# Kernel optimization log

Measured on AMD Instinct MI355X. Metric: run time of the kernel, lower is better.

The kernel has to match this reference:

```python
import jax, jax.numpy as jnp
import numpy as np

D_MODEL = 1024
NUM_HEADS = 16
HEAD_DIM = D_MODEL // NUM_HEADS
B, S = 4, 2048


def setup_inputs() -> dict:
    key = jax.random.key(0)
    ks = jax.random.split(key, 11)
    sc = 1.0 / np.sqrt(D_MODEL)
    return {
        "query": jax.random.normal(ks[0], (B, S, D_MODEL), jnp.float32),
        "key": jax.random.normal(ks[1], (B, S, D_MODEL), jnp.float32),
        "value": jax.random.normal(ks[2], (B, S, D_MODEL), jnp.float32),
        "Wq": jax.random.normal(ks[3], (D_MODEL, D_MODEL), jnp.float32) * sc,
        "bq": jnp.zeros((D_MODEL,), jnp.float32),
        "Wk": jax.random.normal(ks[4], (D_MODEL, D_MODEL), jnp.float32) * sc,
        "bk": jnp.zeros((D_MODEL,), jnp.float32),
        "Wv": jax.random.normal(ks[5], (D_MODEL, D_MODEL), jnp.float32) * sc,
        "bv": jnp.zeros((D_MODEL,), jnp.float32),
        "Wo": jax.random.normal(ks[6], (D_MODEL, D_MODEL), jnp.float32) * sc,
        "bo": jnp.zeros((D_MODEL,), jnp.float32),
    }


def _split_heads(x):
    b, s, _ = x.shape
    return x.reshape(b, s, NUM_HEADS, HEAD_DIM).transpose(0, 2, 1, 3)  # [B,H,S,Dh]


def reference(query, key, value, Wq, bq, Wk, bk, Wv, bv, Wo, bo):
    q = _split_heads(query @ Wq + bq)
    k = _split_heads(key @ Wk + bk)
    v = _split_heads(value @ Wv + bv)
    scores = jnp.einsum("bhqd,bhkd->bhqk", q, k) / np.sqrt(HEAD_DIM)
    attn = jax.nn.softmax(scores, axis=-1)
    out = jnp.einsum("bhqk,bhkd->bhqd", attn, v)
    out = out.transpose(0, 2, 1, 3).reshape(query.shape[0], -1, D_MODEL)
    return out @ Wo + bo
```

## Files before the change

kernel.cpp:

```cpp
#include <hip/hip_runtime.h>

typedef unsigned short u16;
typedef unsigned int   u32;
typedef unsigned long long u64;
typedef __attribute__((ext_vector_type(8))) short bf16x8;
typedef __attribute__((ext_vector_type(4))) float f32x4;

#define S_  2048
#define DH  64
#define DM  1024
#define BS  8192
#define CS  0.18033688011112042f

static __device__ __forceinline__ float bf2f(u16 v){ return __uint_as_float(((u32)v)<<16); }
static __device__ __forceinline__ u16 f2bf(float f){
  u32 x = __float_as_uint(f);
  return (u16)((x + 0x7fffu + ((x>>16)&1u)) >> 16);
}
#if __has_builtin(__builtin_amdgcn_cvt_pk_bf16_f32)
static __device__ __forceinline__ u32 pk2(float x, float y){
  typedef __attribute__((ext_vector_type(2))) __bf16 bf2v;
  union { bf2v v; u32 u; } c; c.v = __builtin_amdgcn_cvt_pk_bf16_f32(x, y); return c.u;
}
#else
static __device__ __forceinline__ u32 pk2(float x, float y){
  return (u32)f2bf(x) | ((u32)f2bf(y) << 16);
}
#endif
#if __has_builtin(__builtin_amdgcn_exp2f)
#define EXP2F(x) __builtin_amdgcn_exp2f(x)
#else
#define EXP2F(x) exp2f(x)
#endif

static __device__ __forceinline__ void dma16(const u16* g, const u16* l){
  __builtin_amdgcn_global_load_lds(
      (const __attribute__((address_space(1))) u32*)(u64)(uintptr_t)g,
      (__attribute__((address_space(3))) u32*)(u32)(u64)(uintptr_t)l, 16, 0, 0);
}

static __device__ __forceinline__ bf16x8 lds_frag(const u16* p){
  union { bf16x8 f; uint2 u[2]; } w;
  w.u[0] = *(const uint2*)(p);
  w.u[1] = *(const uint2*)(p+4);
  return w.f;
}
static __device__ __forceinline__ bf16x8 frag16v(const u16* p){
  union { bf16x8 f; uint4 u; } w;
  w.u = *(const uint4*)p;
  return w.f;
}
static __device__ __forceinline__ void stage16_bf(const u16* __restrict__ g, u16* s){
  uint4 a = *(const uint4*)g;
  uint4 b = *(const uint4*)(g+8);
  *(uint2*)(s+0)  = make_uint2(a.x,a.y);
  *(uint2*)(s+4)  = make_uint2(a.z,a.w);
  *(uint2*)(s+8)  = make_uint2(b.x,b.y);
  *(uint2*)(s+12) = make_uint2(b.z,b.w);
}
static __device__ __forceinline__ void stage16_f32(const float* __restrict__ g, u16* s){
  float4 a0 = ((const float4*)g)[0];
  float4 a1 = ((const float4*)g)[1];
  float4 a2 = ((const float4*)g)[2];
  float4 a3 = ((const float4*)g)[3];
  *(uint2*)(s+0)  = make_uint2(pk2(a0.x,a0.y), pk2(a0.z,a0.w));
  *(uint2*)(s+4)  = make_uint2(pk2(a1.x,a1.y), pk2(a1.z,a1.w));
  *(uint2*)(s+8)  = make_uint2(pk2(a2.x,a2.y), pk2(a2.z,a2.w));
  *(uint2*)(s+12) = make_uint2(pk2(a3.x,a3.y), pk2(a3.z,a3.w));
}

__global__ __launch_bounds__(256) void prep(
    const void* __restrict__ w0, const void* __restrict__ w1,
    const void* __restrict__ w2, const void* __restrict__ w3,
    u16* t0, u16* t1, u16* t2, u16* t3,
    const void* __restrict__ a0, const void* __restrict__ a1,
    const void* __restrict__ a2,
    u16* c0, u16* c1, u16* c2, const int f32f){
  __shared__ u16 tile[32][33];
  int z = blockIdx.z;
  int tid = threadIdx.x;
  bool f32 = f32f != 0;
  if (z < 4){
    const void* in = z==0?w0 : z==1?w1 : z==2?w2 : w3;
    u16* out = z==0?t0 : z==1?t1 : z==2?t2 : t3;
    int tx = tid & 31, ty = tid >> 5;
    int c  = blockIdx.x*32 + tx;
    int r0 = blockIdx.y*32;
    for (int i=ty;i<32;i+=8){
      long off = (long)(r0+i)*DM + c;
      tile[i][tx] = f32 ? f2bf(((const float*)in)[off]) : ((const u16*)in)[off];
    }
    __syncthreads();
    int rr = r0 + tx, cb = blockIdx.x*32;
    for (int i=ty;i<32;i+=8) out[(long)(cb+i)*DM + rr] = tile[tx][i];
  } else {
    if (!f32) return;
    const void* in = z==4?a0 : z==5?a1 : a2;
    u16* out = z==4?c0 : z==5?c1 : c2;
    long lb = (long)blockIdx.y*32 + blockIdx.x;
    long base = (lb*256 + tid)*8;
    #pragma unroll
    for (int it=0; it<4; it++){
      long i = base + (long)it*2097152;
      const float4* p = (const float4*)((const float*)in + i);
      float4 x = p[0], y = p[1];
      *(uint4*)(out + i) = make_uint4(pk2(x.x,x.y), pk2(x.z,x.w), pk2(y.x,y.y), pk2(y.z,y.w));
    }
  }
}

template<int ADMA>
__global__ __launch_bounds__(256) void gemm_qkv(
    const void* __restrict__ A0, const void* __restrict__ A1, const void* __restrict__ A2,
    const u16* __restrict__ W0, const u16* __restrict__ W1, const u16* __restrict__ W2,
    const void* __restrict__ bv0, const void* __restrict__ bv1, const void* __restrict__ bv2,
    u16* C0, u16* C1, u16* C2, const int f32f){
  constexpr int AST = ADMA ? 32 : 36;
  constexpr int NB  = ADMA ? 2 : 1;
  __shared__ __align__(16) u16 As[NB][128*AST];
  __shared__ __align__(16) u16 Bs[NB][128*32];
  int z = blockIdx.z;
  const void* A  = z==0?A0 : z==1?A1 : A2;
  const u16* BT  = z==0?W0 : z==1?W1 : W2;
  const void* bias = z==0?bv0 : z==1?bv1 : bv2;
  u16* C = z==0?C0 : z==1?C1 : C2;
  const bool aF32 = (!ADMA) && (f32f != 0);
  const bool bF32 = (f32f != 0);
  int tid = threadIdx.x;
  int bx = blockIdx.y;
  int lane = tid & 63, w = tid >> 6;
  int t = lane & 15, q = lane >> 4;
  int wr = w >> 1, wc = w & 1;

  const u16* gB = BT + ((long)(bx*128 + w*32 + (lane>>2))*DM + (lane&3)*8);
  float scale = (z==0) ? CS : 1.0f;

  for (int sub = 0; sub < 2; ++sub){
    int by = blockIdx.x*2 + sub;
    f32x4 acc[4][4];
    #pragma unroll
    for(int i=0;i<4;i++) for(int j=0;j<4;j++) for(int k=0;k<4;k++) acc[i][j][k]=0.f;

    if constexpr (ADMA){
      const u16* gA = (const u16*)A + ((long)(by*128 + w*32 + (lane>>2))*DM + (lane&3)*8);
      const int lb = (w*32)*32;
      dma16(gA,         &As[0][lb]);
      dma16(gA + 16*DM, &As[0][lb + 16*32]);
      dma16(gB,         &Bs[0][lb]);
      dma16(gB + 16*DM, &Bs[0][lb + 16*32]);
      for (int k0=0; k0<DM; k0+=32){
        int cur = (k0>>5)&1;
        if (k0+32 < DM){
          dma16(gA + k0+32,         &As[cur^1][lb]);
          dma16(gA + k0+32 + 16*DM, &As[cur^1][lb + 16*32]);
          dma16(gB + k0+32,         &Bs[cur^1][lb]);
          dma16(gB + k0+32 + 16*DM, &Bs[cur^1][lb + 16*32]);
          asm volatile("s_waitcnt vmcnt(4)" ::: "memory");
        } else {
          asm volatile("s_waitcnt vmcnt(0)" ::: "memory");
        }
        __builtin_amdgcn_s_barrier();
        bf16x8 af[4], bfr[4];
        const u16* Ar = &As[cur][(wr*64 + t)*32 + q*8];
        const u16* Br = &Bs[cur][(wc*64 + t)*32 + q*8];
        #pragma unroll
        for (int rt=0;rt<4;rt++) af[rt]  = frag16v(Ar + rt*16*32);
        #pragma unroll
        for (int ct=0;ct<4;ct++) bfr[ct] = frag16v(Br + ct*16*32);
        #pragma unroll
        for (int rt=0;rt<4;rt++)
          #pragma unroll
          for (int ct=0;ct<4;ct++)
            acc[rt][ct] = __builtin_amdgcn_mfma_f32_16x16x32_bf16(af[rt], bfr[ct], acc[rt][ct], 0,0,0);
        __builtin_amdgcn_s_barrier();
      }
    } else {
      long aoff = (long)(by*128 + (tid>>1))*DM + (tid&1)*16;
      const u16* ArdB = &As[0][(wr*64 + t)*AST + q*8];
      const u16* BrdB = &Bs[0][(wc*64 + t)*32  + q*8];
      for (int k0=0; k0<DM; k0+=32){
        dma16(gB + k0,         &Bs[0][(w*32)*32]);
        dma16(gB + 16*DM + k0, &Bs[0][(w*32)*32 + 16*32]);
        u16* AsW = &As[0][(tid>>1)*36 + (tid&1)*16];
        if (aF32) stage16_f32((const float*)A + aoff + k0, AsW);
        else      stage16_bf ((const u16*)A  + aoff + k0, AsW);
        __syncthreads();
        bf16x8 af[4], bfr[4];
        #pragma unroll
        for (int rt=0;rt<4;rt++) af[rt]  = lds_frag(ArdB + rt*16*AST);
        #pragma unroll
        for (int ct=0;ct<4;ct++) bfr[ct] = lds_frag(BrdB + ct*16*32);
        #pragma unroll
        for (int rt=0;rt<4;rt++)
          #pragma unroll
          for (int ct=0;ct<4;ct++)
            acc[rt][ct] = __builtin_amdgcn_mfma_f32_16x16x32_bf16(af[rt], bfr[ct], acc[rt][ct], 0,0,0);
        __syncthreads();
      }
    }

    #pragma unroll
    for (int ct=0;ct<4;ct++){
      int col = bx*128 + wc*64 + ct*16 + t;
      float bvv = bF32 ? ((const float*)bias)[col] : bf2f(((const u16*)bias)[col]);
      #pragma unroll
      for (int rt=0;rt<4;rt++){
        int row0 = by*128 + wr*64 + rt*16 + q*4;
        if (z == 2){
          int bb = row0 >> 11, s = row0 & 2047;
          long vbase = (long)bb*2097152 + (long)col*2048
                     + (s & ~63) + ((rt>>1)<<5) + (q<<3) + ((rt&1)<<2);
          u32 lo = pk2(acc[rt][ct][0]+bvv, acc[rt][ct][1]+bvv);
          u32 hi = pk2(acc[rt][ct][2]+bvv, acc[rt][ct][3]+bvv);
          *(uint2*)(C + vbase) = make_uint2(lo,hi);
        } else {
          #pragma unroll
          for (int r=0;r<4;r++)
            C[(long)(row0+r)*DM + col] = f2bf((acc[rt][ct][r] + bvv)*scale);
        }
      }
    }
  }
}

__global__ __launch_bounds__(256) void gemm_o(const u16* __restrict__ A,
    const u16* __restrict__ BT, const void* __restrict__ bias, void* __restrict__ C,
    const int f32f){
  __shared__ __align__(16) u16 As[2][128*32];
  __shared__ __align__(16) u16 Bs[2][128*32];
  const int f = f32f;
  int tid = threadIdx.x;
  int by = blockIdx.x, bx = blockIdx.y;
  int lane = tid & 63, w = tid >> 6;
  int t = lane & 15, q = lane >> 4;
  int wr = w >> 1, wc = w & 1;
  f32x4 acc[4][4];
  #pragma unroll
  for(int i=0;i<4;i++) for(int j=0;j<4;j++) for(int k=0;k<4;k++) acc[i][j][k]=0.f;

  const u16* gA = A  + ((long)(by*128 + w*32 + (lane>>2))*DM + (lane&3)*8);
  const u16* gB = BT + ((long)(bx*128 + w*32 + (lane>>2))*DM + (lane&3)*8);
  const int lb = (w*32)*32;
  dma16(gA,         &As[0][lb]);
  dma16(gA + 16*DM, &As[0][lb + 16*32]);
  dma16(gB,         &Bs[0][lb]);
  dma16(gB + 16*DM, &Bs[0][lb + 16*32]);
  for (int k0=0; k0<DM; k0+=32){
    int cur = (k0>>5)&1;
    if (k0+32 < DM){
      dma16(gA + k0+32,         &As[cur^1][lb]);
      dma16(gA + k0+32 + 16*DM, &As[cur^1][lb + 16*32]);
      dma16(gB + k0+32,         &Bs[cur^1][lb]);
      dma16(gB + k0+32 + 16*DM, &Bs[cur^1][lb + 16*32]);
      asm volatile("s_waitcnt vmcnt(4)" ::: "memory");
    } else {
      asm volatile("s_waitcnt vmcnt(0)" ::: "memory");
    }
    __builtin_amdgcn_s_barrier();
    bf16x8 af[4], bfr[4];
    const u16* Ar = &As[cur][(wr*64 + t)*32 + q*8];
    const u16* Br = &Bs[cur][(wc*64 + t)*32 + q*8];
    #pragma unroll
    for (int rt=0;rt<4;rt++) af[rt]  = frag16v(Ar + rt*16*32);
    #pragma unroll
    for (int ct=0;ct<4;ct++) bfr[ct] = frag16v(Br + ct*16*32);
    #pragma unroll
    for (int rt=0;rt<4;rt++)
      #pragma unroll
      for (int ct=0;ct<4;ct++)
        acc[rt][ct] = __builtin_amdgcn_mfma_f32_16x16x32_bf16(af[rt], bfr[ct], acc[rt][ct], 0,0,0);
    __builtin_amdgcn_s_barrier();
  }
  #pragma unroll
  for (int ct=0;ct<4;ct++){
    int col = bx*128 + wc*64 + ct*16 + t;
    float bvv = f ? ((const float*)bias)[col] : bf2f(((const u16*)bias)[col]);
    #pragma unroll
    for (int rt=0;rt<4;rt++){
      int row0 = by*128 + wr*64 + rt*16 + q*4;
      #pragma unroll
      for (int r=0;r<4;r++){
        long idx = (long)(row0+r)*DM + col;
        float v = acc[rt][ct][r] + bvv;
        if (f) ((float*)C)[idx] = v;
        else   ((u16*)C)[idx]  = f2bf(v);
      }
    }
  }
}

__global__ __launch_bounds__(256,4) void attn5(const u16* __restrict__ Q,
    const u16* __restrict__ Kb, const u16* __restrict__ Vt, u16* __restrict__ O){
  __shared__ __align__(16) u16 Ks[2][4096];
  __shared__ __align__(16) u16 Vs[2][4096];
  int tid = threadIdx.x;
  int bid = blockIdx.x;
  int qt = bid >> 6;
  int s6 = bid & 63;
  int bh = (s6 & 7)*8 + (s6 >> 3);
  int b = bh >> 4, h = bh & 15;
  int lane = tid & 63, w = tid >> 6;
  int t = lane & 15, q = lane >> 4;

  const u16* Qbase = Q + ((long)(b*S_ + qt*128 + w*32 + t)*DM + h*DH + q*8);
  bf16x8 qf[2][2];
  qf[0][0] = frag16v(Qbase);
  qf[0][1] = frag16v(Qbase + 32);
  qf[1][0] = frag16v(Qbase + 16*DM);
  qf[1][1] = frag16v(Qbase + 16*DM + 32);

  int r0 = tid >> 3;
  int cb = ((tid & 7) * 16) ^ ((r0 & 7) << 4);
  const char* gK = (const char*)Kb + (((long)(b*S_ + r0)*DM + h*DH) << 1) + cb;
  const char* gV = (const char*)Vt + ((((long)bh << 17) + ((long)r0 << 11)) << 1) + cb;
  const long gK1 = ((long)32*DM) << 1;
  const long gV1 = ((long)32*S_) << 1;
  const int ld0 = w*512, ld1 = 2048 + w*512;

  f32x4 o[2][4];
  #pragma unroll
  for (int i=0;i<2;i++) for (int j=0;j<4;j++) for (int k=0;k<4;k++) o[i][j][k]=0.f;
  f32x4 o4[2];
  #pragma unroll
  for (int i=0;i<2;i++) for (int k=0;k<4;k++) o4[i][k]=0.f;

  union { bf16x8 f; u32 u[4]; } vone;
  { u32 ovv = (t==0) ? 0x3F803F80u : 0u;
    vone.u[0]=ovv; vone.u[1]=ovv; vone.u[2]=ovv; vone.u[3]=ovv; }

  const int xorv = (t & 7) << 4;

  dma16((const u16*)(gK),       &Ks[0][ld0]);
  dma16((const u16*)(gK + gK1), &Ks[0][ld1]);
  dma16((const u16*)(gV),       &Vs[0][ld0]);
  dma16((const u16*)(gV + gV1), &Vs[0][ld1]);

  for (int kt=0; kt<32; kt++){
    int cur = kt & 1;
    if (kt < 31){
      long ko = ((long)(kt+1)*64*DM) << 1;
      long vo = (long)(kt+1) << 7;
      dma16((const u16*)(gK + ko),       &Ks[cur^1][ld0]);
      dma16((const u16*)(gK + ko + gK1), &Ks[cur^1][ld1]);
      dma16((const u16*)(gV + vo),       &Vs[cur^1][ld0]);
      dma16((const u16*)(gV + vo + gV1), &Vs[cur^1][ld1]);
      asm volatile("s_waitcnt vmcnt(4)" ::: "memory");
    } else {
      asm volatile("s_waitcnt vmcnt(0)" ::: "memory");
    }
    __builtin_amdgcn_s_barrier();

    const u16* Kc = Ks[cur];
    const u16* Vc = Vs[cur];

    f32x4 sacc[2][4];
    #pragma unroll
    for (int i=0;i<2;i++) for (int j=0;j<4;j++) for (int k=0;k<4;k++) sacc[i][j][k]=0.f;
    #pragma unroll
    for (int ks=0; ks<2; ks++){
      int off = ((ks*64 + q*16) ^ xorv) >> 1;
      bf16x8 k0 = frag16v(Kc + (t     )*64 + off);
      bf16x8 k1 = frag16v(Kc + (16 + t)*64 + off);
      bf16x8 k2 = frag16v(Kc + (32 + t)*64 + off);
      bf16x8 k3 = frag16v(Kc + (48 + t)*64 + off);
      __builtin_amdgcn_s_setprio(1);
      #pragma unroll
      for (int rt=0; rt<2; rt++){
        sacc[rt][0] = __builtin_amdgcn_mfma_f32_16x16x32_bf16(k0, qf[rt][ks], sacc[rt][0],0,0,0);
        sacc[rt][1] = __builtin_amdgcn_mfma_f32_16x16x32_bf16(k1, qf[rt][ks], sacc[rt][1],0,0,0);
        sacc[rt][2] = __builtin_amdgcn_mfma_f32_16x16x32_bf16(k2, qf[rt][ks], sacc[rt][2],0,0,0);
        sacc[rt][3] = __builtin_amdgcn_mfma_f32_16x16x32_bf16(k3, qf[rt][ks], sacc[rt][3],0,0,0);
      }
      __builtin_amdgcn_s_setprio(0);
    }

    union { bf16x8 f; u32 u[4]; } af[2][2];
    #pragma unroll
    for (int rt=0; rt<2; rt++){
      float ev[4][4];
      #pragma unroll
      for (int c=0; c<4; c++)
        #pragma unroll
        for (int r=0; r<4; r++) ev[c][r] = EXP2F(sacc[rt][c][r]);
      #pragma unroll
      for (int ks=0; ks<2; ks++){
        af[rt][ks].u[0] = pk2(ev[2*ks  ][0], ev[2*ks  ][1]);
        af[rt][ks].u[1] = pk2(ev[2*ks  ][2], ev[2*ks  ][3]);
        af[rt][ks].u[2] = pk2(ev[2*ks+1][0], ev[2*ks+1][1]);
        af[rt][ks].u[3] = pk2(ev[2*ks+1][2], ev[2*ks+1][3]);
      }
    }

    #pragma unroll
    for (int ks=0; ks<2; ks++){
      int off = ((ks*64 + q*16) ^ xorv) >> 1;
      bf16x8 v0 = frag16v(Vc + (t     )*64 + off);
      bf16x8 v1 = frag16v(Vc + (16 + t)*64 + off);
      bf16x8 v2 = frag16v(Vc + (32 + t)*64 + off);
      bf16x8 v3 = frag16v(Vc + (48 + t)*64 + off);
      __builtin_amdgcn_s_setprio(1);
      #pragma unroll
      for (int rt=0; rt<2; rt++){
        o[rt][0] = __builtin_amdgcn_mfma_f32_16x16x32_bf16(af[rt][ks].f, v0, o[rt][0],0,0,0);
        o[rt][1] = __builtin_amdgcn_mfma_f32_16x16x32_bf16(af[rt][ks].f, v1, o[rt][1],0,0,0);
        o[rt][2] = __builtin_amdgcn_mfma_f32_16x16x32_bf16(af[rt][ks].f, v2, o[rt][2],0,0,0);
        o[rt][3] = __builtin_amdgcn_mfma_f32_16x16x32_bf16(af[rt][ks].f, v3, o[rt][3],0,0,0);
        o4[rt]   = __builtin_amdgcn_mfma_f32_16x16x32_bf16(af[rt][ks].f, vone.f, o4[rt],0,0,0);
      }
      __builtin_amdgcn_s_setprio(0);
    }
    __builtin_amdgcn_s_barrier();
  }

  #pragma unroll
  for (int rt=0; rt<2; rt++){
    #pragma unroll
    for (int r=0; r<4; r++){
      float l = __shfl(o4[rt][r], lane & 48);
      float inv = 1.f / l;
      int row = qt*128 + w*32 + rt*16 + q*4 + r;
      #pragma unroll
      for (int ct=0; ct<4; ct++)
        O[(long)(b*S_ + row)*DM + h*DH + ct*16 + t] = f2bf(o[rt][ct][r] * inv);
    }
  }
}

extern "C" void kernel_launch(void* const* d_in, const int* in_sizes, int n_in,
                              void* d_out, int out_size, void* d_ws, size_t ws_size,
                              hipStream_t stream){
  (void)n_in; (void)out_size;
  const void* xq = d_in[0];
  const void* xk = d_in[1];
  const void* xv = d_in[2];
  const void* Wq = d_in[3];
  const void* bq = d_in[4];
  const void* Wk = d_in[5];
  const void* bk = d_in[6];
  const void* Wv = d_in[7];
  const void* bv = d_in[8];
  const void* Wo = d_in[9];
  const void* bo = d_in[10];

  const long NT = (long)BS*DM;
  int f32f = 1;
  if (in_sizes && in_sizes[0] == (int)(NT*2)) f32f = 0;

  u16* base = (u16*)((char*)d_ws + 256);
  u16* Qb  = base;
  u16* Kbf = base + NT;
  u16* Vt  = base + 2*NT;
  u16* WqT = base + 3*NT;
  u16* WkT = WqT + (long)DM*DM;
  u16* WvT = WkT + (long)DM*DM;
  u16* WoT = WvT + (long)DM*DM;
  u16* Xc0 = WoT + (long)DM*DM;
  u16* Xc1 = Xc0 + NT;
  u16* Xc2 = Xc1 + NT;
  size_t need_pre = 256 + (size_t)(6*NT + 4*(long)DM*DM)*2;
  bool pre = ws_size >= need_pre;

  dim3 gb(256,1,1);
  int nz = (pre && f32f) ? 7 : 4;
  prep<<<dim3(32,32,nz), gb, 0, stream>>>(Wq, Wk, Wv, Wo,
      WqT, WkT, WvT, WoT, xq, xk, xv, Xc0, Xc1, Xc2, f32f);

  if (pre){
    const void* Aq = f32f ? (const void*)Xc0 : xq;
    const void* Ak = f32f ? (const void*)Xc1 : xk;
    const void* Av = f32f ? (const void*)Xc2 : xv;
    gemm_qkv<1><<<dim3(32,8,3), gb, 0, stream>>>(Aq, Ak, Av,
        WqT, WkT, WvT, bq, bk, bv, Qb, Kbf, Vt, f32f);
  } else {
    gemm_qkv<0><<<dim3(32,8,3), gb, 0, stream>>>(xq, xk, xv,
        WqT, WkT, WvT, bq, bk, bv, Qb, Kbf, Vt, f32f);
  }

  attn5<<<dim3(1024,1,1), gb, 0, stream>>>(Qb, Kbf, Vt, Qb );

  gemm_o<<<dim3(64,8,1), gb, 0, stream>>>(Qb, WoT, bo, d_out, f32f);
}
```

Measured before the change: 383.4 us.

## Swizzle LDS tile layout in GEMMs and drop two-tile loop in QKV GEMM

Changes the global-to-LDS DMA address mapping and fragment read offsets to an XOR-swizzled layout in both the QKV and output-projection GEMMs, aiming to remove LDS bank conflicts on the 16-byte fragment reads. The QKV GEMM no longer loops over two row tiles per block. It launches twice as many blocks (64 instead of 32 in x), one tile each, trading weight-tile reuse for more parallelism. The swizzle must match exactly between the DMA writes and the fragment reads for results to stay correct.

```diff
diff --git a/kernel.cpp b/kernel.cpp
--- a/kernel.cpp
+++ b/kernel.cpp
@@ -127,97 +127,96 @@
   const bool aF32 = (!ADMA) && (f32f != 0);
   const bool bF32 = (f32f != 0);
   int tid = threadIdx.x;
-  int bx = blockIdx.y;
+  int by = blockIdx.x, bx = blockIdx.y;
   int lane = tid & 63, w = tid >> 6;
   int t = lane & 15, q = lane >> 4;
   int wr = w >> 1, wc = w & 1;
-
-  const u16* gB = BT + ((long)(bx*128 + w*32 + (lane>>2))*DM + (lane&3)*8);
+  f32x4 acc[4][4];
+  #pragma unroll
+  for(int i=0;i<4;i++) for(int j=0;j<4;j++) for(int k=0;k<4;k++) acc[i][j][k]=0.f;
+
+  if constexpr (ADMA){
+    int sl = (lane & 7) ^ (lane >> 3);
+    int srow = ((lane >> 3) << 1) + (sl >> 2);
+    const u16* gA = (const u16*)A + ((long)(by*128 + w*32 + srow)*DM + (sl&3)*8);
+    const u16* gB = BT            + ((long)(bx*128 + w*32 + srow)*DM + (sl&3)*8);
+    const int lb = w*1024;
+    int rdo = ((t>>1)<<6) + (((((t&1)<<2) | q) ^ (t>>1)) << 3);
+    dma16(gA,         &As[0][lb]);
+    dma16(gA + 16*DM, &As[0][lb + 512]);
+    dma16(gB,         &Bs[0][lb]);
+    dma16(gB + 16*DM, &Bs[0][lb + 512]);
+    for (int k0=0; k0<DM; k0+=32){
+      int cur = (k0>>5)&1;
+      if (k0+32 < DM){
+        dma16(gA + k0+32,         &As[cur^1][lb]);
+        dma16(gA + k0+32 + 16*DM, &As[cur^1][lb + 512]);
+        dma16(gB + k0+32,         &Bs[cur^1][lb]);
+        dma16(gB + k0+32 + 16*DM, &Bs[cur^1][lb + 512]);
+        asm volatile("s_waitcnt vmcnt(4)" ::: "memory");
+      } else {
+        asm volatile("s_waitcnt vmcnt(0)" ::: "memory");
+      }
+      __builtin_amdgcn_s_barrier();
+      bf16x8 af[4], bfr[4];
+      const u16* Ar = &As[cur][wr*2048 + rdo];
+      const u16* Br = &Bs[cur][wc*2048 + rdo];
+      #pragma unroll
+      for (int rt=0;rt<4;rt++) af[rt]  = frag16v(Ar + rt*512);
+      #pragma unroll
+      for (int ct=0;ct<4;ct++) bfr[ct] = frag16v(Br + ct*512);
+      #pragma unroll
+      for (int rt=0;rt<4;rt++)
+        #pragma unroll
+        for (int ct=0;ct<4;ct++)
+          acc[rt][ct] = __builtin_amdgcn_mfma_f32_16x16x32_bf16(af[rt], bfr[ct], acc[rt][ct], 0,0,0);
+      __builtin_amdgcn_s_barrier();
+    }
+  } else {
+    const u16* gB = BT + ((long)(bx*128 + w*32 + (lane>>2))*DM + (lane&3)*8);
+    long aoff = (long)(by*128 + (tid>>1))*DM + (tid&1)*16;
+    const u16* ArdB = &As[0][(wr*64 + t)*AST + q*8];
+    const u16* BrdB = &Bs[0][(wc*64 + t)*32  + q*8];
+    for (int k0=0; k0<DM; k0+=32){
+      dma16(gB + k0,         &Bs[0][w*1024]);
+      dma16(gB + 16*DM + k0, &Bs[0][w*1024 + 512]);
+      u16* AsW = &As[0][(tid>>1)*36 + (tid&1)*16];
+      if (aF32) stage16_f32((const float*)A + aoff + k0, AsW);
+      else      stage16_bf ((const u16*)A  + aoff + k0, AsW);
+      __syncthreads();
+      bf16x8 af[4], bfr[4];
+      #pragma unroll
+      for (int rt=0;rt<4;rt++) af[rt]  = lds_frag(ArdB + rt*16*AST);
+      #pragma unroll
+      for (int ct=0;ct<4;ct++) bfr[ct] = lds_frag(BrdB + ct*16*32);
+      #pragma unroll
+      for (int rt=0;rt<4;rt++)
+        #pragma unroll
+        for (int ct=0;ct<4;ct++)
+          acc[rt][ct] = __builtin_amdgcn_mfma_f32_16x16x32_bf16(af[rt], bfr[ct], acc[rt][ct], 0,0,0);
+      __syncthreads();
+    }
+  }
+
   float scale = (z==0) ? CS : 1.0f;
-
-  for (int sub = 0; sub < 2; ++sub){
-    int by = blockIdx.x*2 + sub;
-    f32x4 acc[4][4];
-    #pragma unroll
-    for(int i=0;i<4;i++) for(int j=0;j<4;j++) for(int k=0;k<4;k++) acc[i][j][k]=0.f;
-
-    if constexpr (ADMA){
-      const u16* gA = (const u16*)A + ((long)(by*128 + w*32 + (lane>>2))*DM + (lane&3)*8);
-      const int lb = (w*32)*32;
-      dma16(gA,         &As[0][lb]);
-      dma16(gA + 16*DM, &As[0][lb + 16*32]);
-      dma16(gB,         &Bs[0][lb]);
-      dma16(gB + 16*DM, &Bs[0][lb + 16*32]);
-      for (int k0=0; k0<DM; k0+=32){
-        int cur = (k0>>5)&1;
-        if (k0+32 < DM){
-          dma16(gA + k0+32,         &As[cur^1][lb]);
-          dma16(gA + k0+32 + 16*DM, &As[cur^1][lb + 16*32]);
-          dma16(gB + k0+32,         &Bs[cur^1][lb]);
-          dma16(gB + k0+32 + 16*DM, &Bs[cur^1][lb + 16*32]);
-          asm volatile("s_waitcnt vmcnt(4)" ::: "memory");
-        } else {
-          asm volatile("s_waitcnt vmcnt(0)" ::: "memory");
-        }
-        __builtin_amdgcn_s_barrier();
-        bf16x8 af[4], bfr[4];
-        const u16* Ar = &As[cur][(wr*64 + t)*32 + q*8];
-        const u16* Br = &Bs[cur][(wc*64 + t)*32 + q*8];
+  #pragma unroll
+  for (int ct=0;ct<4;ct++){
+    int col = bx*128 + wc*64 + ct*16 + t;
+    float bvv = bF32 ? ((const float*)bias)[col] : bf2f(((const u16*)bias)[col]);
+    #pragma unroll
+    for (int rt=0;rt<4;rt++){
+      int row0 = by*128 + wr*64 + rt*16 + q*4;
+      if (z == 2){
+        int bb = row0 >> 11, s = row0 & 2047;
+        long vbase = (long)bb*2097152 + (long)col*2048
+                   + (s & ~63) + ((rt>>1)<<5) + (q<<3) + ((rt&1)<<2);
+        u32 lo = pk2(acc[rt][ct][0]+bvv, acc[rt][ct][1]+bvv);
+        u32 hi = pk2(acc[rt][ct][2]+bvv, acc[rt][ct][3]+bvv);
+        *(uint2*)(C + vbase) = make_uint2(lo,hi);
+      } else {
         #pragma unroll
-        for (int rt=0;rt<4;rt++) af[rt]  = frag16v(Ar + rt*16*32);
-        #pragma unroll
-        for (int ct=0;ct<4;ct++) bfr[ct] = frag16v(Br + ct*16*32);
-        #pragma unroll
-        for (int rt=0;rt<4;rt++)
-          #pragma unroll
-          for (int ct=0;ct<4;ct++)
-            acc[rt][ct] = __builtin_amdgcn_mfma_f32_16x16x32_bf16(af[rt], bfr[ct], acc[rt][ct], 0,0,0);
-        __builtin_amdgcn_s_barrier();
-      }
-    } else {
-      long aoff = (long)(by*128 + (tid>>1))*DM + (tid&1)*16;
-      const u16* ArdB = &As[0][(wr*64 + t)*AST + q*8];
-      const u16* BrdB = &Bs[0][(wc*64 + t)*32  + q*8];
-      for (int k0=0; k0<DM; k0+=32){
-        dma16(gB + k0,         &Bs[0][(w*32)*32]);
-        dma16(gB + 16*DM + k0, &Bs[0][(w*32)*32 + 16*32]);
-        u16* AsW = &As[0][(tid>>1)*36 + (tid&1)*16];
-        if (aF32) stage16_f32((const float*)A + aoff + k0, AsW);
-        else      stage16_bf ((const u16*)A  + aoff + k0, AsW);
-        __syncthreads();
-        bf16x8 af[4], bfr[4];
-        #pragma unroll
-        for (int rt=0;rt<4;rt++) af[rt]  = lds_frag(ArdB + rt*16*AST);
-        #pragma unroll
-        for (int ct=0;ct<4;ct++) bfr[ct] = lds_frag(BrdB + ct*16*32);
-        #pragma unroll
-        for (int rt=0;rt<4;rt++)
-          #pragma unroll
-          for (int ct=0;ct<4;ct++)
-            acc[rt][ct] = __builtin_amdgcn_mfma_f32_16x16x32_bf16(af[rt], bfr[ct], acc[rt][ct], 0,0,0);
-        __syncthreads();
-      }
-    }
-
-    #pragma unroll
-    for (int ct=0;ct<4;ct++){
-      int col = bx*128 + wc*64 + ct*16 + t;
-      float bvv = bF32 ? ((const float*)bias)[col] : bf2f(((const u16*)bias)[col]);
-      #pragma unroll
-      for (int rt=0;rt<4;rt++){
-        int row0 = by*128 + wr*64 + rt*16 + q*4;
-        if (z == 2){
-          int bb = row0 >> 11, s = row0 & 2047;
-          long vbase = (long)bb*2097152 + (long)col*2048
-                     + (s & ~63) + ((rt>>1)<<5) + (q<<3) + ((rt&1)<<2);
-          u32 lo = pk2(acc[rt][ct][0]+bvv, acc[rt][ct][1]+bvv);
-          u32 hi = pk2(acc[rt][ct][2]+bvv, acc[rt][ct][3]+bvv);
-          *(uint2*)(C + vbase) = make_uint2(lo,hi);
-        } else {
-          #pragma unroll
-          for (int r=0;r<4;r++)
-            C[(long)(row0+r)*DM + col] = f2bf((acc[rt][ct][r] + bvv)*scale);
-        }
+        for (int r=0;r<4;r++)
+          C[(long)(row0+r)*DM + col] = f2bf((acc[rt][ct][r] + bvv)*scale);
       }
     }
   }
@@ -238,32 +237,35 @@
   #pragma unroll
   for(int i=0;i<4;i++) for(int j=0;j<4;j++) for(int k=0;k<4;k++) acc[i][j][k]=0.f;
 
-  const u16* gA = A  + ((long)(by*128 + w*32 + (lane>>2))*DM + (lane&3)*8);
-  const u16* gB = BT + ((long)(bx*128 + w*32 + (lane>>2))*DM + (lane&3)*8);
-  const int lb = (w*32)*32;
+  int sl = (lane & 7) ^ (lane >> 3);
+  int srow = ((lane >> 3) << 1) + (sl >> 2);
+  const u16* gA = A  + ((long)(by*128 + w*32 + srow)*DM + (sl&3)*8);
+  const u16* gB = BT + ((long)(bx*128 + w*32 + srow)*DM + (sl&3)*8);
+  const int lb = w*1024;
+  int rdo = ((t>>1)<<6) + (((((t&1)<<2) | q) ^ (t>>1)) << 3);
   dma16(gA,         &As[0][lb]);
-  dma16(gA + 16*DM, &As[0][lb + 16*32]);
+  dma16(gA + 16*DM, &As[0][lb + 512]);
   dma16(gB,         &Bs[0][lb]);
-  dma16(gB + 16*DM, &Bs[0][lb + 16*32]);
+  dma16(gB + 16*DM, &Bs[0][lb + 512]);
   for (int k0=0; k0<DM; k0+=32){
     int cur = (k0>>5)&1;
     if (k0+32 < DM){
       dma16(gA + k0+32,         &As[cur^1][lb]);
-      dma16(gA + k0+32 + 16*DM, &As[cur^1][lb + 16*32]);
+      dma16(gA + k0+32 + 16*DM, &As[cur^1][lb + 512]);
       dma16(gB + k0+32,         &Bs[cur^1][lb]);
-      dma16(gB + k0+32 + 16*DM, &Bs[cur^1][lb + 16*32]);
+      dma16(gB + k0+32 + 16*DM, &Bs[cur^1][lb + 512]);
       asm volatile("s_waitcnt vmcnt(4)" ::: "memory");
     } else {
       asm volatile("s_waitcnt vmcnt(0)" ::: "memory");
     }
     __builtin_amdgcn_s_barrier();
     bf16x8 af[4], bfr[4];
-    const u16* Ar = &As[cur][(wr*64 + t)*32 + q*8];
-    const u16* Br = &Bs[cur][(wc*64 + t)*32 + q*8];
-    #pragma unroll
-    for (int rt=0;rt<4;rt++) af[rt]  = frag16v(Ar + rt*16*32);
-    #pragma unroll
-    for (int ct=0;ct<4;ct++) bfr[ct] = frag16v(Br + ct*16*32);
+    const u16* Ar = &As[cur][wr*2048 + rdo];
+    const u16* Br = &Bs[cur][wc*2048 + rdo];
+    #pragma unroll
+    for (int rt=0;rt<4;rt++) af[rt]  = frag16v(Ar + rt*512);
+    #pragma unroll
+    for (int ct=0;ct<4;ct++) bfr[ct] = frag16v(Br + ct*512);
     #pragma unroll
     for (int rt=0;rt<4;rt++)
       #pragma unroll
@@ -469,10 +471,10 @@
     const void* Aq = f32f ? (const void*)Xc0 : xq;
     const void* Ak = f32f ? (const void*)Xc1 : xk;
     const void* Av = f32f ? (const void*)Xc2 : xv;
-    gemm_qkv<1><<<dim3(32,8,3), gb, 0, stream>>>(Aq, Ak, Av,
+    gemm_qkv<1><<<dim3(64,8,3), gb, 0, stream>>>(Aq, Ak, Av,
         WqT, WkT, WvT, bq, bk, bv, Qb, Kbf, Vt, f32f);
   } else {
-    gemm_qkv<0><<<dim3(32,8,3), gb, 0, stream>>>(xq, xk, xv,
+    gemm_qkv<0><<<dim3(64,8,3), gb, 0, stream>>>(xq, xk, xv,
         WqT, WkT, WvT, bq, bk, bv, Qb, Kbf, Vt, f32f);
   }
 
```

After: 352.7 us. -8.0%, faster.
